# Kernel tuning notes

Measured on AMD Instinct MI355X. Metric: run time of the kernel, lower is better.

The kernel has to match this reference:

```python
import jax, jax.numpy as jnp
import numpy as np

B, V, K, DIN, H, DH, OBS, HID = 2048, 3, 32, 256, 8, 64, 128, 256
REP = H * DH
EPS = 1e-6


def _ln(x, g, b):
    mu = x.mean(-1, keepdims=True)
    var = ((x - mu) ** 2).mean(-1, keepdims=True)
    return (x - mu) * jax.lax.rsqrt(var + 1e-5) * g + b


def setup_inputs() -> dict:
    key = jax.random.key(0)
    ks = iter(jax.random.split(key, 32))
    nrm = lambda shape, s=0.05: jax.random.normal(next(ks), shape, jnp.float32) * s
    return {
        'x_anchor': jax.random.normal(next(ks), (B, V, DIN), jnp.float32),
        'x_neighbors': jax.random.normal(next(ks), (B, V, K, DIN), jnp.float32),
        'edge_weights': jax.random.uniform(next(ks), (B, V, K), jnp.float32),
        'g': jax.random.normal(next(ks), (B, OBS), jnp.float32),
        'aW': nrm((V, DIN, REP)), 'ab': jnp.zeros((V, REP)), 'ag': jnp.ones((V, REP)), 'abeta': jnp.zeros((V, REP)),
        'nW': nrm((V, DIN, REP)), 'nb': jnp.zeros((V, REP)), 'ng': jnp.ones((V, REP)), 'nbeta': jnp.zeros((V, REP)),
        'Wq': nrm((V, H, DH, DH)), 'Wk': nrm((V, H, DH, DH)), 'Wv': nrm((V, H, DH, DH)), 'Wo': nrm((V, H, DH, DH)),
        'geom_log_scale': jnp.zeros((V, H)),
        'cWq': nrm((H, DH, DH)), 'cWk': nrm((H, DH, DH)), 'cWv': nrm((H, DH, DH)), 'cWo': nrm((H, DH, DH)),
        'rW1': nrm((OBS, HID)), 'rb1': jnp.zeros((HID,)),
        'rW2': nrm((HID, HID)), 'rb2': jnp.zeros((HID,)),
        'vW': nrm((HID, H * V)), 'vb': jnp.zeros((H * V,)),
        'mW': nrm((HID, H)), 'mb': jnp.zeros((H,)),
        'gW': nrm((HID, H)), 'gb': jnp.zeros((H,)),
    }


def reference(x_anchor, x_neighbors, edge_weights, g, aW, ab, ag, abeta, nW, nb, ng, nbeta,
              Wq, Wk, Wv, Wo, geom_log_scale, cWq, cWk, cWv, cWo,
              rW1, rb1, rW2, rb2, vW, vb, mW, mb, gW, gb):
    # --- per-view encoders (vectorized over V with a leading v axis) ---
    ha = _ln(jnp.einsum('bvi,vio->bvo', x_anchor, aW) + ab, ag, abeta).reshape(B, V, H, DH)
    hn = _ln(jnp.einsum('bvki,vio->bvko', x_neighbors, nW) + nb[:, None, :],
             ng[:, None, :], nbeta[:, None, :]).reshape(B, V, K, H, DH)
    q = jnp.einsum('bvhd,vhde->bvhe', ha, Wq)
    k = jnp.einsum('bvkhd,vhde->bvkhe', hn, Wk)
    vv = jnp.einsum('bvkhd,vhde->bvkhe', hn, Wv)
    sc = jnp.einsum('bvhd,bvkhd->bvhk', q, k) / np.sqrt(DH).astype(np.float32)
    geom = jax.nn.softplus(geom_log_scale)  # [V,H]
    sc = sc + geom[None, :, :, None] * jnp.log(edge_weights[:, :, None, :] + EPS)
    attn = jax.nn.softmax(sc, axis=-1)
    ho = jnp.einsum('bvhk,bvkhd->bvhd', attn, vv)
    ho = jnp.einsum('bvhd,vhde->bvhe', ho, Wo) + ha  # residual
    view_tokens = jnp.transpose(ho, (0, 2, 1, 3))  # [B,H,V,Dh]
    # --- router ---
    hid = jax.nn.gelu(jnp.dot(g, rW1) + rb1, approximate=False)
    hid = jax.nn.gelu(jnp.dot(hid, rW2) + rb2, approximate=False)
    pi = jax.nn.softmax((jnp.dot(hid, vW) + vb).reshape(B, H, V), axis=-1)
    beta = jax.nn.sigmoid((jnp.dot(hid, mW) + mb)[..., None])  # [B,H,1]
    gate = jax.nn.softmax(jnp.dot(hid, gW) + gb, axis=-1)      # [B,H]
    # --- pi-weighted mixture + cross-view interaction with log-pi prior ---
    mix = jnp.einsum('bhv,bhvd->bhd', pi, view_tokens)
    qc = jnp.einsum('bhd,hde->bhe', mix, cWq)
    kc = jnp.einsum('bhvd,hde->bhve', view_tokens, cWk)
    vc = jnp.einsum('bhvd,hde->bhve', view_tokens, cWv)
    s2 = jnp.einsum('bhd,bhvd->bhv', qc, kc) / np.sqrt(DH).astype(np.float32) + jnp.log(pi + EPS)
    a2 = jax.nn.softmax(s2, axis=-1)
    cr = jnp.einsum('bhv,bhvd->bhd', a2, vc)
    cr = jnp.einsum('bhd,hde->bhe', cr, cWo)
    # mode blend + head gating; head_repr kept unflattened [B,H,Dh]
    return gate[..., None] * (beta * cr + (1.0 - beta) * mix)
```

## Files before the change

kernel.cpp:

```cpp
#include <hip/hip_runtime.h>

#define B_   2048
#define V_   3
#define K_   32
#define DIN_ 256
#define H_   8
#define DH_  64
#define REP_ 512

typedef unsigned short u16;
typedef unsigned int   u32;
typedef __bf16 bf8 __attribute__((ext_vector_type(8)));
typedef float  f4  __attribute__((ext_vector_type(4)));

static __device__ __forceinline__ u16 f2bf(float f) {
  union { float f; u32 i; } x; x.f = f;
  u32 r = (x.i + 0x7FFFu + ((x.i >> 16) & 1u)) >> 16;
  return (u16)r;
}
static __device__ __forceinline__ float bflo(u32 q) {
  union { u32 i; float f; } x; x.i = q << 16; return x.f;
}
static __device__ __forceinline__ float bfhi(u32 q) {
  union { u32 i; float f; } x; x.i = q & 0xffff0000u; return x.f;
}
static __device__ __forceinline__ u32 pk2bf(float lo, float hi) {
  u32 r;
  asm("v_cvt_pk_bf16_f32 %0, %1, %2" : "=v"(r) : "v"(lo), "v"(hi));
  return r;
}

__global__ __launch_bounds__(256) void k0_fuse(
    const float* __restrict__ nW, const float* __restrict__ aW,
    const float* __restrict__ Wv,
    const float* __restrict__ Wq, const float* __restrict__ Wk,
    u16* __restrict__ nWt, u16* __restrict__ aWt, u16* __restrict__ Wvt,
    float* __restrict__ Wqk)
{
  __shared__ float sm8[8192];
  int bid = blockIdx.x, t = threadIdx.x;
  if (bid < 1536) {
    int id = bid * 256 + t;
    int n = id & 511, k = (id >> 9) & 255, v = id >> 17;
    int kt = k >> 5, k5 = k & 31;
    int dst = ((v * 8 + kt) * 512 + n) * 32 + k5;
    nWt[dst] = f2bf(nW[id]);
    aWt[dst] = f2bf(aW[id]);
  } else if (bid < 1920) {
    int j = (bid - 1536) * 256 + t;
    int vh = j >> 12, r = j & 4095;
    int e = r >> 6, d = r & 63;
    Wvt[j] = f2bf(Wv[(vh * 64 + d) * 64 + e]);
  } else {
    int vh = bid - 1920;
    float* wq = sm8;
    float* wkT = sm8 + 4096;
    #pragma unroll
    for (int i = 0; i < 16; ++i) {
      int idx = i * 256 + t;
      wq[idx] = Wq[(long)vh * 4096 + idx];
      int e = idx >> 6, c = idx & 63;
      wkT[c * 64 + e] = Wk[(long)vh * 4096 + e * 64 + c];
    }
    __syncthreads();
    int d = t >> 2, e0 = (t & 3) * 16;
    float acc[16];
    #pragma unroll
    for (int j = 0; j < 16; ++j) acc[j] = 0.f;
    for (int c = 0; c < 64; ++c) {
      float a = wq[d * 64 + c];
      const float* wr = &wkT[c * 64 + e0];
      #pragma unroll
      for (int j = 0; j < 16; ++j) acc[j] += a * wr[j];
    }
    #pragma unroll
    for (int j = 0; j < 16; ++j) Wqk[(long)vh * 4096 + d * 64 + e0 + j] = acc[j];
  }
}

__global__ __launch_bounds__(256) void k_tq(
    const float* __restrict__ ha, const float* __restrict__ Wqk,
    float* __restrict__ tB)
{
  __shared__ float hs[512];
  int bv = blockIdx.x, t = threadIdx.x;
  int v = bv % 3;
  hs[t]       = ha[(long)bv * 512 + t];
  hs[256 + t] = ha[(long)bv * 512 + 256 + t];
  __syncthreads();
  int h = t >> 5, e0 = (t & 31) * 2;
  const float* wq = Wqk + ((long)v * 8 + h) * 4096 + e0;
  const float* hv = &hs[h * 64];
  float a0 = 0.f, a1 = 0.f;
  #pragma unroll 4
  for (int d = 0; d < 64; ++d) {
    float x = hv[d];
    float2 wv = *(const float2*)&wq[d * 64];
    a0 += x * wv.x;
    a1 += x * wv.y;
  }
  tB[(long)bv * 512 + h * 64 + e0]     = a0 * 0.125f;
  tB[(long)bv * 512 + h * 64 + e0 + 1] = a1 * 0.125f;
}

__global__ __launch_bounds__(512, 4) void k1a_anchor(
    const float* __restrict__ X,
    const u16*   __restrict__ Wt,
    const float* __restrict__ bias,
    const float* __restrict__ gamma,
    const float* __restrict__ betap,
    float* __restrict__ ha)
{
  __shared__ u16 A[64 * 256];
  __shared__ float lnP1[256], lnP2[256], muRs[128];

  const int v = blockIdx.y, blk = blockIdx.x, t = threadIdx.x;
  const int w = t >> 6, l = t & 63, lm = l & 15, lg = l >> 4;
  const int wm = w & 1, wn = w >> 1;

  {
    int row = t >> 3;
    int cbase = (t & 7) * 32;
    int b = blk * 64 + row;
    const float4* src = (const float4*)(X + (long)(b * 3 + v) * 256 + cbase);
    int sw = row & 7;
    #pragma unroll
    for (int j = 0; j < 8; ++j) {
      float4 f = src[j];
      int col = cbase + j * 4;
      int c = col >> 3, m = col & 7;
      uint2 u;
      u.x = pk2bf(f.x, f.y);
      u.y = pk2bf(f.z, f.w);
      *(uint2*)&A[row * 256 + ((c ^ sw) << 3) + m] = u;
    }
  }
  __syncthreads();

  f4 acc[2][8];
  #pragma unroll
  for (int i = 0; i < 2; ++i)
    #pragma unroll
    for (int j = 0; j < 8; ++j) { f4 z = {0.f, 0.f, 0.f, 0.f}; acc[i][j] = z; }

  {
    const u16* Bv = Wt + (long)v * 131072 + ((wn * 128 + lm) * 32 + lg * 8);
    const int row0 = wm * 32 + lm, row1 = row0 + 16;
    #pragma unroll 1
    for (int kt = 0; kt < 8; ++kt) {
      const u16* bp = Bv + kt * 16384;
      bf8 bv[8];
      #pragma unroll
      for (int tn = 0; tn < 8; ++tn) bv[tn] = *(const bf8*)(bp + tn * 512);
      int c = kt * 4 + lg;
      bf8 af0 = *(const bf8*)&A[row0 * 256 + ((c ^ (row0 & 7)) << 3)];
      bf8 af1 = *(const bf8*)&A[row1 * 256 + ((c ^ (row1 & 7)) << 3)];
      #pragma unroll
      for (int tn = 0; tn < 8; ++tn) {
        acc[0][tn] = __builtin_amdgcn_mfma_f32_16x16x32_bf16(bv[tn], af0, acc[0][tn], 0, 0, 0);
        acc[1][tn] = __builtin_amdgcn_mfma_f32_16x16x32_bf16(bv[tn], af1, acc[1][tn], 0, 0, 0);
      }
    }
  }

  #pragma unroll
  for (int tn = 0; tn < 8; ++tn) {
    float4 bb = *(const float4*)&bias[v * 512 + wn * 128 + tn * 16 + lg * 4];
    #pragma unroll
    for (int r = 0; r < 4; ++r) { acc[0][tn][r] += ((const float*)&bb)[r]; acc[1][tn][r] += ((const float*)&bb)[r]; }
  }

  #pragma unroll
  for (int tm = 0; tm < 2; ++tm) {
    float s1 = 0.f, s2 = 0.f;
    #pragma unroll
    for (int tn = 0; tn < 8; ++tn)
      #pragma unroll
      for (int r = 0; r < 4; ++r) { float z = acc[tm][tn][r]; s1 += z; s2 += z * z; }
    s1 += __shfl_xor(s1, 16, 64); s2 += __shfl_xor(s2, 16, 64);
    s1 += __shfl_xor(s1, 32, 64); s2 += __shfl_xor(s2, 32, 64);
    if (lg == 0) {
      int row = wm * 32 + tm * 16 + lm;
      lnP1[row * 4 + wn] = s1;
      lnP2[row * 4 + wn] = s2;
    }
  }
  __syncthreads();
  if (t < 64) {
    float p = lnP1[t * 4] + lnP1[t * 4 + 1] + lnP1[t * 4 + 2] + lnP1[t * 4 + 3];
    float q = lnP2[t * 4] + lnP2[t * 4 + 1] + lnP2[t * 4 + 2] + lnP2[t * 4 + 3];
    float mu = p * (1.f / 512.f);
    float var = q * (1.f / 512.f) - mu * mu;
    muRs[t]      = mu;
    muRs[64 + t] = rsqrtf(var + 1e-5f);
  }
  __syncthreads();

  {
    float mu0 = muRs[wm * 32 + lm],      rs0 = muRs[64 + wm * 32 + lm];
    float mu1 = muRs[wm * 32 + 16 + lm], rs1 = muRs[64 + wm * 32 + 16 + lm];
    int b0g = blk * 64 + wm * 32 + lm, b1g = b0g + 16;
    #pragma unroll
    for (int tn = 0; tn < 8; ++tn) {
      int col0 = wn * 128 + tn * 16 + lg * 4;
      float4 g4 = *(const float4*)&gamma[v * 512 + col0];
      float4 b4 = *(const float4*)&betap[v * 512 + col0];
      float4 y;
      y.x = (acc[0][tn][0] - mu0) * rs0 * g4.x + b4.x;
      y.y = (acc[0][tn][1] - mu0) * rs0 * g4.y + b4.y;
      y.z = (acc[0][tn][2] - mu0) * rs0 * g4.z + b4.z;
      y.w = (acc[0][tn][3] - mu0) * rs0 * g4.w + b4.w;
      *(float4*)&ha[(long)(b0g * 3 + v) * 512 + col0] = y;
      y.x = (acc[1][tn][0] - mu1) * rs1 * g4.x + b4.x;
      y.y = (acc[1][tn][1] - mu1) * rs1 * g4.y + b4.y;
      y.z = (acc[1][tn][2] - mu1) * rs1 * g4.z + b4.z;
      y.w = (acc[1][tn][3] - mu1) * rs1 * g4.w + b4.w;
      *(float4*)&ha[(long)(b1g * 3 + v) * 512 + col0] = y;
    }
  }
}

union K12Smem {
  u16 A[64 * 256];
  u16 S[64 * 512];
};

__global__ __launch_bounds__(512, 4) void k12_fused(
    const float* __restrict__ X,
    const u16*   __restrict__ Wt,
    const float* __restrict__ bias,
    const float* __restrict__ gamma,
    const float* __restrict__ betap,
    const float* __restrict__ ha,
    const u16*   __restrict__ Wvt,
    const float* __restrict__ tB,
    const float* __restrict__ Wo,
    const float* __restrict__ ew,
    const float* __restrict__ gls,
    float* __restrict__ vt)
{
  __shared__ K12Smem sm;
  __shared__ float tS[1024];
  __shared__ float aS[512];
  __shared__ float oSbuf[1024];
  float* lnP1 = oSbuf;
  float* lnP2 = oSbuf + 256;
  float* muRs = oSbuf + 512;

  const int v = blockIdx.y, blk = blockIdx.x, t = threadIdx.x;
  const int w = t >> 6, l = t & 63, lm = l & 15, lg = l >> 4;
  const int wm = w & 1, wn = w >> 1;

  {
    int row = t >> 3;
    int cbase = (t & 7) * 32;
    int b = blk * 2 + (row >> 5);
    long grow = ((long)(b * 3 + v) * 32 + (row & 31)) * 256;
    const float4* src = (const float4*)(X + grow + cbase);
    int sw = row & 7;
    #pragma unroll
    for (int j = 0; j < 8; ++j) {
      float4 f = src[j];
      int col = cbase + j * 4;
      int c = col >> 3, m = col & 7;
      uint2 u;
      u.x = pk2bf(f.x, f.y);
      u.y = pk2bf(f.z, f.w);
      *(uint2*)&sm.A[row * 256 + ((c ^ sw) << 3) + m] = u;
    }
  }
  {
    int b = t >> 8, e = (t & 255) * 2;
    *(float2*)&tS[b * 512 + e] =
        *(const float2*)&tB[((long)(blk * 2 + b) * 3 + v) * 512 + e];
  }
  __syncthreads();

  f4 acc[2][8];
  #pragma unroll
  for (int i = 0; i < 2; ++i)
    #pragma unroll
    for (int j = 0; j < 8; ++j) { f4 z = {0.f, 0.f, 0.f, 0.f}; acc[i][j] = z; }

  {
    const u16* Bv = Wt + (long)v * 131072 + ((wn * 128 + lm) * 32 + lg * 8);
    const int row0 = wm * 32 + lm, row1 = row0 + 16;
    #pragma unroll 1
    for (int kt = 0; kt < 8; ++kt) {
      const u16* bp = Bv + kt * 16384;
      bf8 bv[8];
      #pragma unroll
      for (int tn = 0; tn < 8; ++tn) bv[tn] = *(const bf8*)(bp + tn * 512);
      int c = kt * 4 + lg;
      bf8 af0 = *(const bf8*)&sm.A[row0 * 256 + ((c ^ (row0 & 7)) << 3)];
      bf8 af1 = *(const bf8*)&sm.A[row1 * 256 + ((c ^ (row1 & 7)) << 3)];
      #pragma unroll
      for (int tn = 0; tn < 8; ++tn) {
        acc[0][tn] = __builtin_amdgcn_mfma_f32_16x16x32_bf16(bv[tn], af0, acc[0][tn], 0, 0, 0);
        acc[1][tn] = __builtin_amdgcn_mfma_f32_16x16x32_bf16(bv[tn], af1, acc[1][tn], 0, 0, 0);
      }
    }
  }

  #pragma unroll
  for (int tn = 0; tn < 8; ++tn) {
    float4 bb = *(const float4*)&bias[v * 512 + wn * 128 + tn * 16 + lg * 4];
    #pragma unroll
    for (int r = 0; r < 4; ++r) { acc[0][tn][r] += ((const float*)&bb)[r]; acc[1][tn][r] += ((const float*)&bb)[r]; }
  }

  #pragma unroll
  for (int tm = 0; tm < 2; ++tm) {
    float s1 = 0.f, s2 = 0.f;
    #pragma unroll
    for (int tn = 0; tn < 8; ++tn)
      #pragma unroll
      for (int r = 0; r < 4; ++r) { float z = acc[tm][tn][r]; s1 += z; s2 += z * z; }
    s1 += __shfl_xor(s1, 16, 64); s2 += __shfl_xor(s2, 16, 64);
    s1 += __shfl_xor(s1, 32, 64); s2 += __shfl_xor(s2, 32, 64);
    if (lg == 0) {
      int row = wm * 32 + tm * 16 + lm;
      lnP1[row * 4 + wn] = s1;
      lnP2[row * 4 + wn] = s2;
    }
  }
  __syncthreads();
  if (t < 64) {
    float p = lnP1[t * 4] + lnP1[t * 4 + 1] + lnP1[t * 4 + 2] + lnP1[t * 4 + 3];
    float q = lnP2[t * 4] + lnP2[t * 4 + 1] + lnP2[t * 4 + 2] + lnP2[t * 4 + 3];
    float mu = p * (1.f / 512.f);
    float var = q * (1.f / 512.f) - mu * mu;
    muRs[t]      = mu;
    muRs[64 + t] = rsqrtf(var + 1e-5f);
  }
  __syncthreads();

  {
    float mu0 = muRs[wm * 32 + lm],      rs0 = muRs[64 + wm * 32 + lm];
    float mu1 = muRs[wm * 32 + 16 + lm], rs1 = muRs[64 + wm * 32 + 16 + lm];
    int row0 = wm * 32 + lm, row1 = row0 + 16;
    int sw0 = row0 & 7, sw1 = row1 & 7;
    #pragma unroll
    for (int tn = 0; tn < 8; ++tn) {
      int col0 = wn * 128 + tn * 16 + lg * 4;
      int c = col0 >> 3, m0 = col0 & 7;
      float4 g4 = *(const float4*)&gamma[v * 512 + col0];
      float4 b4 = *(const float4*)&betap[v * 512 + col0];
      {
        float y0 = (acc[0][tn][0] - mu0) * rs0 * g4.x + b4.x;
        float y1 = (acc[0][tn][1] - mu0) * rs0 * g4.y + b4.y;
        float y2 = (acc[0][tn][2] - mu0) * rs0 * g4.z + b4.z;
        float y3 = (acc[0][tn][3] - mu0) * rs0 * g4.w + b4.w;
        uint2 p;
        p.x = pk2bf(y0, y1);
        p.y = pk2bf(y2, y3);
        *(uint2*)&sm.S[row0 * 512 + ((c ^ sw0) << 3) + m0] = p;
      }
      {
        float y0 = (acc[1][tn][0] - mu1) * rs1 * g4.x + b4.x;
        float y1 = (acc[1][tn][1] - mu1) * rs1 * g4.y + b4.y;
        float y2 = (acc[1][tn][2] - mu1) * rs1 * g4.z + b4.z;
        float y3 = (acc[1][tn][3] - mu1) * rs1 * g4.w + b4.w;
        uint2 p;
        p.x = pk2bf(y0, y1);
        p.y = pk2bf(y2, y3);
        *(uint2*)&sm.S[row1 * 512 + ((c ^ sw1) << 3) + m0] = p;
      }
    }
  }
  __syncthreads();

  {
    int b = t >> 8, h = (t >> 5) & 7, k = t & 31;
    float x = gls[v * 8 + h];
    float gsc = (x > 20.f) ? x : log1pf(expf(x));
    int r = b * 32 + k, sw = r & 7;
    const float* tb = &tS[(b * 8 + h) * 64];
    float s = 0.f;
    #pragma unroll
    for (int j = 0; j < 8; ++j) {
      int c8 = h * 8 + j;
      uint4 q = *(const uint4*)&sm.S[r * 512 + ((c8 ^ sw) << 3)];
      const float* tj = tb + j * 8;
      s += tj[0] * bflo(q.x) + tj[1] * bfhi(q.x)
         + tj[2] * bflo(q.y) + tj[3] * bfhi(q.y)
         + tj[4] * bflo(q.z) + tj[5] * bfhi(q.z)
         + tj[6] * bflo(q.w) + tj[7] * bfhi(q.w);
    }
    float e_w = ew[((long)(blk * 2 + b) * 3 + v) * 32 + k];
    s += gsc * logf(e_w + 1e-6f);
    float m = s;
    #pragma unroll
    for (int d = 1; d < 32; d <<= 1) m = fmaxf(m, __shfl_xor(m, d, 64));
    float exs = expf(s - m), sum = exs;
    #pragma unroll
    for (int d = 1; d < 32; d <<= 1) sum += __shfl_xor(sum, d, 64);
    aS[(b * 8 + h) * 32 + k] = exs / sum;
  }
  __syncthreads();

  #pragma unroll 1
  for (int i = 0; i < 2; ++i) {
    int p = w * 2 + i, b = p >> 3, h = p & 7;
    const u16* wvg = Wvt + (long)(v * 8 + h) * 4096;
    f4 aV[2][4];
    #pragma unroll
    for (int a = 0; a < 2; ++a)
      #pragma unroll
      for (int j = 0; j < 4; ++j) { f4 z = {0.f, 0.f, 0.f, 0.f}; aV[a][j] = z; }
    #pragma unroll
    for (int ks = 0; ks < 2; ++ks) {
      int ko = ks * 32 + lg * 8;
      bf8 af[2];
      #pragma unroll
      for (int tm = 0; tm < 2; ++tm) {
        int r = b * 32 + tm * 16 + lm;
        int c8 = h * 8 + ks * 4 + lg;
        af[tm] = *(const bf8*)&sm.S[r * 512 + ((c8 ^ (r & 7)) << 3)];
      }
      #pragma unroll
      for (int tn = 0; tn < 4; ++tn) {
        bf8 bv = *(const bf8*)&wvg[(tn * 16 + lm) * 64 + ko];
        #pragma unroll
        for (int tm = 0; tm < 2; ++tm)
          aV[tm][tn] = __builtin_amdgcn_mfma_f32_16x16x32_bf16(af[tm], bv, aV[tm][tn], 0, 0, 0);
      }
    }
    float pp[4] = {0.f, 0.f, 0.f, 0.f};
    #pragma unroll
    for (int tm = 0; tm < 2; ++tm)
      #pragma unroll
      for (int r4 = 0; r4 < 4; ++r4) {
        int k = tm * 16 + lg * 4 + r4;
        float a = aS[p * 32 + k];
        #pragma unroll
        for (int tn = 0; tn < 4; ++tn) pp[tn] += a * aV[tm][tn][r4];
      }
    #pragma unroll
    for (int tn = 0; tn < 4; ++tn) {
      float x = pp[tn];
      x += __shfl_xor(x, 16, 64);
      x += __shfl_xor(x, 32, 64);
      if (l < 16) oSbuf[p * 64 + tn * 16 + lm] = x;
    }
  }
  __syncthreads();

  {
    int h = t >> 6, e = t & 63;
    const float* wo = Wo + (long)(v * 8 + h) * 4096;
    float a0 = ha[((long)(blk * 2 + 0) * 3 + v) * 512 + h * 64 + e];
    float a1 = ha[((long)(blk * 2 + 1) * 3 + v) * 512 + h * 64 + e];
    const float* o0 = &oSbuf[h * 64];
    const float* o1 = &oSbuf[512 + h * 64];
    #pragma unroll 8
    for (int d = 0; d < 64; ++d) {
      float wv = wo[d * 64 + e];
      a0 += o0[d] * wv;
      a1 += o1[d] * wv;
    }
    vt[(((long)(blk * 2 + 0) * 8 + h) * 3 + v) * 64 + e] = a0;
    vt[(((long)(blk * 2 + 1) * 8 + h) * 3 + v) * 64 + e] = a1;
  }
}

__global__ __launch_bounds__(256) void k34_router_cross(
    const float* __restrict__ g,
    const float* __restrict__ rW1, const float* __restrict__ rb1,
    const float* __restrict__ rW2, const float* __restrict__ rb2,
    const float* __restrict__ vW, const float* __restrict__ vb,
    const float* __restrict__ mW, const float* __restrict__ mb,
    const float* __restrict__ gW, const float* __restrict__ gb,
    const float* __restrict__ vtg,
    const float* __restrict__ cWq, const float* __restrict__ cWk,
    const float* __restrict__ cWv, const float* __restrict__ cWo,
    float* __restrict__ out)
{
  __shared__ float smem[12544];
  __shared__ float gs[512], h1[1024], h2[1024], lgt[160];
  float* vts   = smem;
  float* mixs  = smem + 6144;
  float* buf1  = smem + 8192;
  float* buf2  = smem + 10240;
  float* a2s   = smem + 12288;
  float* pis   = smem + 12384;
  float* betas = smem + 12480;
  float* gates = smem + 12512;

  int t = threadIdx.x, bb = blockIdx.x * 4;

  {
    const float4* src = (const float4*)(vtg + (long)bb * 1536);
    #pragma unroll
    for (int r = 0; r < 6; ++r) ((float4*)vts)[r * 256 + t] = src[r * 256 + t];
    gs[t]       = g[(long)bb * 128 + t];
    gs[256 + t] = g[(long)bb * 128 + 256 + t];
  }
  __syncthreads();

  {
    int bl = t >> 6, e0 = (t & 63) * 4;
    float acc[4];
    #pragma unroll
    for (int j = 0; j < 4; ++j) acc[j] = rb1[e0 + j];
    for (int i = 0; i < 128; ++i) {
      float gv = gs[bl * 128 + i];
      const float* wr = rW1 + i * 256 + e0;
      #pragma unroll
      for (int j = 0; j < 4; ++j) acc[j] += gv * wr[j];
    }
    #pragma unroll
    for (int j = 0; j < 4; ++j) { float x = acc[j]; h1[bl * 256 + e0 + j] = 0.5f * x * (1.f + erff(x * 0.70710678118f)); }
  }
  __syncthreads();
  {
    int bl = t >> 6, e0 = (t & 63) * 4;
    float acc[4];
    #pragma unroll
    for (int j = 0; j < 4; ++j) acc[j] = rb2[e0 + j];
    for (int i = 0; i < 256; ++i) {
      float hv = h1[bl * 256 + i];
      const float* wr = rW2 + i * 256 + e0;
      #pragma unroll
      for (int j = 0; j < 4; ++j) acc[j] += hv * wr[j];
    }
    #pragma unroll
    for (int j = 0; j < 4; ++j) { float x = acc[j]; h2[bl * 256 + e0 + j] = 0.5f * x * (1.f + erff(x * 0.70710678118f)); }
  }
  __syncthreads();
  if (t < 160) {
    int bl = t / 40, j = t % 40;
    const float* W; float bs; int col, stride;
    if (j < 24)      { W = vW; col = j;      stride = 24; bs = vb[j]; }
    else if (j < 32) { W = mW; col = j - 24; stride = 8;  bs = mb[j - 24]; }
    else             { W = gW; col = j - 32; stride = 8;  bs = gb[j - 32]; }
    float acc = bs;
    for (int i = 0; i < 256; ++i) acc += h2[bl * 256 + i] * W[i * stride + col];
    lgt[bl * 40 + j] = acc;
  }
  __syncthreads();
  if (t < 4) {
    const float* L = &lgt[t * 40];
    #pragma unroll
    for (int hh = 0; hh < 8; ++hh) {
      float a0 = L[hh * 3], a1 = L[hh * 3 + 1], a2v = L[hh * 3 + 2];
      float m = fmaxf(a0, fmaxf(a1, a2v));
      float x0 = expf(a0 - m), x1 = expf(a1 - m), x2 = expf(a2v - m);
      float inv = 1.f / (x0 + x1 + x2);
      pis[t * 24 + hh * 3 + 0] = x0 * inv;
      pis[t * 24 + hh * 3 + 1] = x1 * inv;
      pis[t * 24 + hh * 3 + 2] = x2 * inv;
      betas[t * 8 + hh] = 1.f / (1.f + expf(-L[24 + hh]));
    }
    float m = L[32];
    #pragma unroll
    for (int hh = 1; hh < 8; ++hh) m = fmaxf(m, L[32 + hh]);
    float s = 0.f, ex[8];
    #pragma unroll
    for (int hh = 0; hh < 8; ++hh) { ex[hh] = expf(L[32 + hh] - m); s += ex[hh]; }
    float inv = 1.f / s;
    #pragma unroll
    for (int hh = 0; hh < 8; ++hh) gates[t * 8 + hh] = ex[hh] * inv;
  }
  __syncthreads();

  int bl = t >> 6, hh = (t >> 3) & 7, e0 = (t & 7) * 8;
  const float* vbh = &vts[(bl * 8 + hh) * 192];
  {
    float p0 = pis[bl * 24 + hh * 3], p1 = pis[bl * 24 + hh * 3 + 1], p2 = pis[bl * 24 + hh * 3 + 2];
    #pragma unroll
    for (int j = 0; j < 8; ++j) {
      int e = e0 + j;
      mixs[(bl * 8 + hh) * 64 + e] = p0 * vbh[e] + p1 * vbh[64 + e] + p2 * vbh[128 + e];
    }
  }
  __syncthreads();
  {
    float acc[8] = {0.f,0.f,0.f,0.f,0.f,0.f,0.f,0.f};
    const float* M = &mixs[(bl * 8 + hh) * 64];
    for (int d = 0; d < 64; ++d) {
      float mv = M[d];
      const float* wr = &cWq[(hh * 64 + d) * 64 + e0];
      #pragma unroll
      for (int j = 0; j < 8; ++j) acc[j] += mv * wr[j];
    }
    #pragma unroll
    for (int j = 0; j < 8; ++j) buf1[(bl * 8 + hh) * 64 + e0 + j] = acc[j] * 0.125f;
  }
  __syncthreads();
  {
    const float* Q = &buf1[(bl * 8 + hh) * 64];
    #pragma unroll
    for (int d2 = 0; d2 < 8; ++d2) {
      const float* wr = &cWk[(hh * 64 + e0 + d2) * 64];
      float a = 0.f;
      for (int e = 0; e < 64; ++e) a += wr[e] * Q[e];
      buf2[(bl * 8 + hh) * 64 + e0 + d2] = a;
    }
  }
  __syncthreads();
  if (t < 32) {
    int b2 = t >> 3, h2 = t & 7;
    const float* Wd = &buf2[(b2 * 8 + h2) * 64];
    const float* vb2 = &vts[(b2 * 8 + h2) * 192];
    float s[3];
    #pragma unroll
    for (int v3 = 0; v3 < 3; ++v3) {
      float a = 0.f;
      for (int d = 0; d < 64; ++d) a += Wd[d] * vb2[v3 * 64 + d];
      s[v3] = a + logf(pis[b2 * 24 + h2 * 3 + v3] + 1e-6f);
    }
    float m = fmaxf(s[0], fmaxf(s[1], s[2]));
    float x0 = expf(s[0] - m), x1 = expf(s[1] - m), x2 = expf(s[2] - m);
    float inv = 1.f / (x0 + x1 + x2);
    a2s[(b2 * 8 + h2) * 3 + 0] = x0 * inv;
    a2s[(b2 * 8 + h2) * 3 + 1] = x1 * inv;
    a2s[(b2 * 8 + h2) * 3 + 2] = x2 * inv;
  }
  __syncthreads();
  {
    float a0 = a2s[(bl * 8 + hh) * 3], a1 = a2s[(bl * 8 + hh) * 3 + 1], a2v = a2s[(bl * 8 + hh) * 3 + 2];
    #pragma unroll
    for (int j = 0; j < 8; ++j) {
      int e = e0 + j;
      buf1[(bl * 8 + hh) * 64 + e] = a0 * vbh[e] + a1 * vbh[64 + e] + a2v * vbh[128 + e];
    }
  }
  __syncthreads();
  {
    float acc[8] = {0.f,0.f,0.f,0.f,0.f,0.f,0.f,0.f};
    const float* Y = &buf1[(bl * 8 + hh) * 64];
    for (int d = 0; d < 64; ++d) {
      float yv = Y[d];
      const float* wr = &cWv[(hh * 64 + d) * 64 + e0];
      #pragma unroll
      for (int j = 0; j < 8; ++j) acc[j] += yv * wr[j];
    }
    #pragma unroll
    for (int j = 0; j < 8; ++j) buf2[(bl * 8 + hh) * 64 + e0 + j] = acc[j];
  }
  __syncthreads();
  {
    float acc[8] = {0.f,0.f,0.f,0.f,0.f,0.f,0.f,0.f};
    const float* C2 = &buf2[(bl * 8 + hh) * 64];
    for (int d = 0; d < 64; ++d) {
      float cv = C2[d];
      const float* wr = &cWo[(hh * 64 + d) * 64 + e0];
      #pragma unroll
      for (int j = 0; j < 8; ++j) acc[j] += cv * wr[j];
    }
    float bt = betas[bl * 8 + hh], gt = gates[bl * 8 + hh];
    const float* M = &mixs[(bl * 8 + hh) * 64];
    #pragma unroll
    for (int j = 0; j < 8; ++j)
      out[((long)(bb + bl) * 8 + hh) * 64 + e0 + j] = gt * (bt * acc[j] + (1.f - bt) * M[e0 + j]);
  }
}

extern "C" void kernel_launch(void* const* d_in, const int* in_sizes, int n_in,
                              void* d_out, int out_size, void* d_ws, size_t ws_size,
                              hipStream_t stream) {
  const float* x_anchor    = (const float*)d_in[0];
  const float* x_neighbors = (const float*)d_in[1];
  const float* edge_w      = (const float*)d_in[2];
  const float* g           = (const float*)d_in[3];
  const float* aW  = (const float*)d_in[4];
  const float* ab  = (const float*)d_in[5];
  const float* ag  = (const float*)d_in[6];
  const float* abeta = (const float*)d_in[7];
  const float* nW  = (const float*)d_in[8];
  const float* nb  = (const float*)d_in[9];
  const float* ng  = (const float*)d_in[10];
  const float* nbeta = (const float*)d_in[11];
  const float* Wq  = (const float*)d_in[12];
  const float* Wk  = (const float*)d_in[13];
  const float* Wv  = (const float*)d_in[14];
  const float* Wo  = (const float*)d_in[15];
  const float* gls = (const float*)d_in[16];
  const float* cWq = (const float*)d_in[17];
  const float* cWk = (const float*)d_in[18];
  const float* cWv = (const float*)d_in[19];
  const float* cWo = (const float*)d_in[20];
  const float* rW1 = (const float*)d_in[21];
  const float* rb1 = (const float*)d_in[22];
  const float* rW2 = (const float*)d_in[23];
  const float* rb2 = (const float*)d_in[24];
  const float* vW  = (const float*)d_in[25];
  const float* vb  = (const float*)d_in[26];
  const float* mW  = (const float*)d_in[27];
  const float* mb  = (const float*)d_in[28];
  const float* gW  = (const float*)d_in[29];
  const float* gb  = (const float*)d_in[30];

  char* p = (char*)d_ws;
  u16* nWt = (u16*)p;  p += 786432;
  u16* aWt = (u16*)p;  p += 786432;
  u16* Wvt = (u16*)p;  p += 196608;
  float* WqkB = (float*)p; p += 393216;
  float* ha   = (float*)p; p += 12582912;
  float* vtb  = (float*)p; p += 12582912;
  float* tqB  = (float*)p; p += 12582912;
  (void)ws_size;

  k0_fuse<<<1944, 256, 0, stream>>>(nW, aW, Wv, Wq, Wk, nWt, aWt, Wvt, WqkB);
  k1a_anchor<<<dim3(32, 3), 512, 0, stream>>>(x_anchor, aWt, ab, ag, abeta, ha);
  k_tq<<<6144, 256, 0, stream>>>(ha, WqkB, tqB);
  k12_fused<<<dim3(1024, 3), 512, 0, stream>>>(x_neighbors, nWt, nb, ng, nbeta,
                                               ha, Wvt, tqB, Wo, edge_w, gls, vtb);
  k34_router_cross<<<512, 256, 0, stream>>>(g, rW1, rb1, rW2, rb2, vW, vb,
                                            mW, mb, gW, gb, vtb,
                                            cWq, cWk, cWv, cWo, (float*)d_out);
}
```

Before: 785.2 us.

## Stage weight tiles through swizzled LDS with register prefetch in encoder GEMMs

The weight pre-pack now writes a bank-swizzled k-tile layout. Both encoder GEMM kernels (anchor and neighbor) then copy each 32-wide k-slice of the weights cooperatively into LDS, prefetching the next slice into registers while the current one is consumed by MFMAs. Before, each wave loaded its own B fragments directly from global memory. Each weight slice is now fetched once per block instead of once per wave row-group, at the cost of 32KB of extra LDS, two barriers per k-step, and possibly lower occupancy.

```diff
diff --git a/kernel.cpp b/kernel.cpp
--- a/kernel.cpp
+++ b/kernel.cpp
@@ -41,11 +41,16 @@
   int bid = blockIdx.x, t = threadIdx.x;
   if (bid < 1536) {
     int id = bid * 256 + t;
-    int n = id & 511, k = (id >> 9) & 255, v = id >> 17;
-    int kt = k >> 5, k5 = k & 31;
-    int dst = ((v * 8 + kt) * 512 + n) * 32 + k5;
-    nWt[dst] = f2bf(nW[id]);
-    aWt[dst] = f2bf(aW[id]);
+    int v  = id / 131072, r  = id % 131072;
+    int kt = r / 16384,   r2 = r % 16384;
+    int n  = r2 >> 5;
+    int s  = (r2 >> 3) & 3;
+    int m  = r2 & 7;
+    int c  = s ^ ((n >> 1) & 3);
+    int k  = kt * 32 + c * 8 + m;
+    int src = (v * 256 + k) * 512 + n;
+    nWt[id] = f2bf(nW[src]);
+    aWt[id] = f2bf(aW[src]);
   } else if (bid < 1920) {
     int j = (bid - 1536) * 256 + t;
     int vh = j >> 12, r = j & 4095;
@@ -112,11 +117,21 @@
     float* __restrict__ ha)
 {
   __shared__ u16 A[64 * 256];
+  __shared__ u16 Bt[16384];
   __shared__ float lnP1[256], lnP2[256], muRs[128];
 
   const int v = blockIdx.y, blk = blockIdx.x, t = threadIdx.x;
   const int w = t >> 6, l = t & 63, lm = l & 15, lg = l >> 4;
   const int wm = w & 1, wn = w >> 1;
+
+  const u16* Wbase = Wt + (long)v * 131072;
+
+  uint4 pf[4];
+  {
+    const uint4* gp = (const uint4*)(Wbase + t * 8);
+    #pragma unroll
+    for (int r = 0; r < 4; ++r) pf[r] = gp[r * 512];
+  }
 
   {
     int row = t >> 3;
@@ -135,7 +150,6 @@
       *(uint2*)&A[row * 256 + ((c ^ sw) << 3) + m] = u;
     }
   }
-  __syncthreads();
 
   f4 acc[2][8];
   #pragma unroll
@@ -143,23 +157,31 @@
     #pragma unroll
     for (int j = 0; j < 8; ++j) { f4 z = {0.f, 0.f, 0.f, 0.f}; acc[i][j] = z; }
 
-  {
-    const u16* Bv = Wt + (long)v * 131072 + ((wn * 128 + lm) * 32 + lg * 8);
-    const int row0 = wm * 32 + lm, row1 = row0 + 16;
-    #pragma unroll 1
-    for (int kt = 0; kt < 8; ++kt) {
-      const u16* bp = Bv + kt * 16384;
-      bf8 bv[8];
-      #pragma unroll
-      for (int tn = 0; tn < 8; ++tn) bv[tn] = *(const bf8*)(bp + tn * 512);
+  for (int kt = 0; kt < 8; ++kt) {
+    __syncthreads();
+    *(uint4*)&Bt[t * 8]         = pf[0];
+    *(uint4*)&Bt[t * 8 + 4096]  = pf[1];
+    *(uint4*)&Bt[t * 8 + 8192]  = pf[2];
+    *(uint4*)&Bt[t * 8 + 12288] = pf[3];
+    __syncthreads();
+    if (kt < 7) {
+      const uint4* gp = (const uint4*)(Wbase + (kt + 1) * 16384 + t * 8);
+      #pragma unroll
+      for (int r = 0; r < 4; ++r) pf[r] = gp[r * 512];
+    }
+    bf8 af[2];
+    #pragma unroll
+    for (int tm = 0; tm < 2; ++tm) {
+      int row = wm * 32 + tm * 16 + lm;
       int c = kt * 4 + lg;
-      bf8 af0 = *(const bf8*)&A[row0 * 256 + ((c ^ (row0 & 7)) << 3)];
-      bf8 af1 = *(const bf8*)&A[row1 * 256 + ((c ^ (row1 & 7)) << 3)];
-      #pragma unroll
-      for (int tn = 0; tn < 8; ++tn) {
-        acc[0][tn] = __builtin_amdgcn_mfma_f32_16x16x32_bf16(bv[tn], af0, acc[0][tn], 0, 0, 0);
-        acc[1][tn] = __builtin_amdgcn_mfma_f32_16x16x32_bf16(bv[tn], af1, acc[1][tn], 0, 0, 0);
-      }
+      af[tm] = *(const bf8*)&A[row * 256 + ((c ^ (row & 7)) << 3)];
+    }
+    #pragma unroll
+    for (int tn = 0; tn < 8; ++tn) {
+      int n = wn * 128 + tn * 16 + lm;
+      bf8 bv = *(const bf8*)&Bt[n * 32 + ((lg ^ ((n >> 1) & 3)) << 3)];
+      acc[0][tn] = __builtin_amdgcn_mfma_f32_16x16x32_bf16(bv, af[0], acc[0][tn], 0, 0, 0);
+      acc[1][tn] = __builtin_amdgcn_mfma_f32_16x16x32_bf16(bv, af[1], acc[1][tn], 0, 0, 0);
     }
   }
 
@@ -221,7 +243,7 @@
 }
 
 union K12Smem {
-  u16 A[64 * 256];
+  struct { u16 A[64 * 256]; u16 Bt[16384]; } p;
   u16 S[64 * 512];
 };
 
@@ -251,6 +273,15 @@
   const int w = t >> 6, l = t & 63, lm = l & 15, lg = l >> 4;
   const int wm = w & 1, wn = w >> 1;
 
+  const u16* Wbase = Wt + (long)v * 131072;
+
+  uint4 pf[4];
+  {
+    const uint4* gp = (const uint4*)(Wbase + t * 8);
+    #pragma unroll
+    for (int r = 0; r < 4; ++r) pf[r] = gp[r * 512];
+  }
+
   {
     int row = t >> 3;
     int cbase = (t & 7) * 32;
@@ -266,7 +297,7 @@
       uint2 u;
       u.x = pk2bf(f.x, f.y);
       u.y = pk2bf(f.z, f.w);
-      *(uint2*)&sm.A[row * 256 + ((c ^ sw) << 3) + m] = u;
+      *(uint2*)&sm.p.A[row * 256 + ((c ^ sw) << 3) + m] = u;
     }
   }
   {
@@ -274,7 +305,6 @@
     *(float2*)&tS[b * 512 + e] =
         *(const float2*)&tB[((long)(blk * 2 + b) * 3 + v) * 512 + e];
   }
-  __syncthreads();
 
   f4 acc[2][8];
   #pragma unroll
@@ -282,23 +312,31 @@
     #pragma unroll
     for (int j = 0; j < 8; ++j) { f4 z = {0.f, 0.f, 0.f, 0.f}; acc[i][j] = z; }
 
-  {
-    const u16* Bv = Wt + (long)v * 131072 + ((wn * 128 + lm) * 32 + lg * 8);
-    const int row0 = wm * 32 + lm, row1 = row0 + 16;
-    #pragma unroll 1
-    for (int kt = 0; kt < 8; ++kt) {
-      const u16* bp = Bv + kt * 16384;
-      bf8 bv[8];
-      #pragma unroll
-      for (int tn = 0; tn < 8; ++tn) bv[tn] = *(const bf8*)(bp + tn * 512);
+  for (int kt = 0; kt < 8; ++kt) {
+    __syncthreads();
+    *(uint4*)&sm.p.Bt[t * 8]         = pf[0];
+    *(uint4*)&sm.p.Bt[t * 8 + 4096]  = pf[1];
+    *(uint4*)&sm.p.Bt[t * 8 + 8192]  = pf[2];
+    *(uint4*)&sm.p.Bt[t * 8 + 12288] = pf[3];
+    __syncthreads();
+    if (kt < 7) {
+      const uint4* gp = (const uint4*)(Wbase + (kt + 1) * 16384 + t * 8);
+      #pragma unroll
+      for (int r = 0; r < 4; ++r) pf[r] = gp[r * 512];
+    }
+    bf8 af[2];
+    #pragma unroll
+    for (int tm = 0; tm < 2; ++tm) {
+      int row = wm * 32 + tm * 16 + lm;
       int c = kt * 4 + lg;
-      bf8 af0 = *(const bf8*)&sm.A[row0 * 256 + ((c ^ (row0 & 7)) << 3)];
-      bf8 af1 = *(const bf8*)&sm.A[row1 * 256 + ((c ^ (row1 & 7)) << 3)];
-      #pragma unroll
-      for (int tn = 0; tn < 8; ++tn) {
-        acc[0][tn] = __builtin_amdgcn_mfma_f32_16x16x32_bf16(bv[tn], af0, acc[0][tn], 0, 0, 0);
-        acc[1][tn] = __builtin_amdgcn_mfma_f32_16x16x32_bf16(bv[tn], af1, acc[1][tn], 0, 0, 0);
-      }
+      af[tm] = *(const bf8*)&sm.p.A[row * 256 + ((c ^ (row & 7)) << 3)];
+    }
+    #pragma unroll
+    for (int tn = 0; tn < 8; ++tn) {
+      int n = wn * 128 + tn * 16 + lm;
+      bf8 bv = *(const bf8*)&sm.p.Bt[n * 32 + ((lg ^ ((n >> 1) & 3)) << 3)];
+      acc[0][tn] = __builtin_amdgcn_mfma_f32_16x16x32_bf16(bv, af[0], acc[0][tn], 0, 0, 0);
+      acc[1][tn] = __builtin_amdgcn_mfma_f32_16x16x32_bf16(bv, af[1], acc[1][tn], 0, 0, 0);
     }
   }
 
```

Result: slower. 900.4 us (+14.7%).
